# Kernel optimization log

Hardware: AMD Instinct MI355X
Metric: run time of the kernel (lower is better)

## Reference

```python
import jax, jax.numpy as jnp
import numpy as np

TEMPERATURE = 1.0
ITERATIONS = 5


def setup_inputs() -> dict:
    key = jax.random.key(0)
    logits = jax.random.normal(key, (64, 1024, 1024), dtype=jnp.float32)
    return {"logits": logits}


def reference(logits) -> jnp.ndarray:
    # Sinkhorn-Knopp in log space: alternate row and column log-normalization.
    def body(log_alpha, _):
        log_alpha = log_alpha - jax.nn.logsumexp(log_alpha, axis=2, keepdims=True)
        log_alpha = log_alpha - jax.nn.logsumexp(log_alpha, axis=1, keepdims=True)
        return log_alpha, None

    log_alpha, _ = jax.lax.scan(body, logits, None, length=ITERATIONS)
    return jnp.exp(log_alpha / TEMPERATURE)
```

## Files before the change

kernel.cpp:

```cpp
#include <hip/hip_runtime.h>


constexpr int BATCH = 64;
constexpr int N = 1024;
constexpr int ROWS_PER_WAVE = 16;
constexpr int WAVES_PER_WG = 4;
constexpr int PASS_BLOCKS = (BATCH * N) / (ROWS_PER_WAVE * WAVES_PER_WG);
constexpr int FINAL_BLOCKS = 16384;

__global__ __launch_bounds__(256) void init_ws_kernel(float* __restrict__ v,
                                                      float* __restrict__ colsum) {
    int t = blockIdx.x * blockDim.x + threadIdx.x;
    v[t] = 0.0f;
    colsum[t] = 0.0f;
}

__global__ __launch_bounds__(256) void sinkhorn_pass_kernel(
    const float* __restrict__ logits, const float* __restrict__ v,
    float* __restrict__ u, float* __restrict__ colsum) {
    __shared__ float lds[WAVES_PER_WG * N];

    const int tid = threadIdx.x;
    const int lane = tid & 63;
    const int wid = tid >> 6;
    const int wave_g = blockIdx.x * WAVES_PER_WG + wid;
    const int row0 = wave_g * ROWS_PER_WAVE;
    const int b = row0 >> 10;

    const float4* vb = reinterpret_cast<const float4*>(v + (b << 10));
    float4 vr[4];
#pragma unroll
    for (int c = 0; c < 4; ++c) vr[c] = vb[c * 64 + lane];

    float4 acc[4];
#pragma unroll
    for (int c = 0; c < 4; ++c) acc[c] = make_float4(0.f, 0.f, 0.f, 0.f);

    const float4* lb =
        reinterpret_cast<const float4*>(logits) + (size_t)row0 * (N / 4) + lane;

    for (int ii = 0; ii < ROWS_PER_WAVE; ++ii) {
        float4 x[4];
#pragma unroll
        for (int c = 0; c < 4; ++c) x[c] = lb[ii * (N / 4) + c * 64];
#pragma unroll
        for (int c = 0; c < 4; ++c) {
            x[c].x -= vr[c].x;
            x[c].y -= vr[c].y;
            x[c].z -= vr[c].z;
            x[c].w -= vr[c].w;
        }
        float m = x[0].x;
#pragma unroll
        for (int c = 0; c < 4; ++c) {
            m = fmaxf(m, x[c].x);
            m = fmaxf(m, x[c].y);
            m = fmaxf(m, x[c].z);
            m = fmaxf(m, x[c].w);
        }
#pragma unroll
        for (int off = 32; off >= 1; off >>= 1) m = fmaxf(m, __shfl_xor(m, off));
        float s = 0.f;
#pragma unroll
        for (int c = 0; c < 4; ++c) {
            x[c].x = __expf(x[c].x - m); s += x[c].x;
            x[c].y = __expf(x[c].y - m); s += x[c].y;
            x[c].z = __expf(x[c].z - m); s += x[c].z;
            x[c].w = __expf(x[c].w - m); s += x[c].w;
        }
#pragma unroll
        for (int off = 32; off >= 1; off >>= 1) s += __shfl_xor(s, off);
        if (lane == 0) u[row0 + ii] = m + __logf(s);
        const float rinv = __builtin_amdgcn_rcpf(s);
#pragma unroll
        for (int c = 0; c < 4; ++c) {
            acc[c].x = fmaf(x[c].x, rinv, acc[c].x);
            acc[c].y = fmaf(x[c].y, rinv, acc[c].y);
            acc[c].z = fmaf(x[c].z, rinv, acc[c].z);
            acc[c].w = fmaf(x[c].w, rinv, acc[c].w);
        }
    }
#pragma unroll
    for (int c = 0; c < 4; ++c) {
        acc[c].x *= __expf(vr[c].x);
        acc[c].y *= __expf(vr[c].y);
        acc[c].z *= __expf(vr[c].z);
        acc[c].w *= __expf(vr[c].w);
    }
    float4* lw = reinterpret_cast<float4*>(lds + wid * N);
#pragma unroll
    for (int c = 0; c < 4; ++c) lw[c * 64 + lane] = acc[c];
    __syncthreads();

    const int j0 = tid * 4;
    float4 s0 = *reinterpret_cast<const float4*>(lds + 0 * N + j0);
    const float4 s1 = *reinterpret_cast<const float4*>(lds + 1 * N + j0);
    const float4 s2 = *reinterpret_cast<const float4*>(lds + 2 * N + j0);
    const float4 s3 = *reinterpret_cast<const float4*>(lds + 3 * N + j0);
    s0.x += s1.x + s2.x + s3.x;
    s0.y += s1.y + s2.y + s3.y;
    s0.z += s1.z + s2.z + s3.z;
    s0.w += s1.w + s2.w + s3.w;
    float* dst = colsum + (b << 10) + j0;
    atomicAdd(dst + 0, s0.x);
    atomicAdd(dst + 1, s0.y);
    atomicAdd(dst + 2, s0.z);
    atomicAdd(dst + 3, s0.w);
}

__global__ __launch_bounds__(256) void finalize_kernel(float* __restrict__ colsum,
                                                       float* __restrict__ v) {
    int t = blockIdx.x * blockDim.x + threadIdx.x;
    v[t] = __logf(colsum[t]);
    colsum[t] = 0.0f;
}

__global__ __launch_bounds__(256) void final_kernel(const float* __restrict__ logits,
                                                    const float* __restrict__ u,
                                                    const float* __restrict__ v,
                                                    float* __restrict__ out) {
    const int g0 = blockIdx.x * 256 + threadIdx.x;
#pragma unroll
    for (int p = 0; p < 4; ++p) {
        const int g = g0 + p * (FINAL_BLOCKS * 256);
        const int e = g << 2;
        const int r = e >> 10;
        const int jc = e & 1023;
        const int b = r >> 10;
        const float ur = u[r];
        const float4 vv = *reinterpret_cast<const float4*>(v + (b << 10) + jc);
        const float4 x = *reinterpret_cast<const float4*>(logits + (size_t)e);
        float4 o;
        o.x = __expf(x.x - ur - vv.x);
        o.y = __expf(x.y - ur - vv.y);
        o.z = __expf(x.z - ur - vv.z);
        o.w = __expf(x.w - ur - vv.w);
        *reinterpret_cast<float4*>(out + (size_t)e) = o;
    }
}

extern "C" void kernel_launch(void* const* d_in, const int* in_sizes, int n_in,
                              void* d_out, int out_size, void* d_ws, size_t ws_size,
                              hipStream_t stream) {
    const float* logits = (const float*)d_in[0];
    float* out = (float*)d_out;
    float* ws = (float*)d_ws;
    float* u = ws;
    float* v = ws + 65536;
    float* colsum = ws + 131072;

    init_ws_kernel<<<256, 256, 0, stream>>>(v, colsum);
    for (int it = 0; it < 5; ++it) {
        sinkhorn_pass_kernel<<<PASS_BLOCKS, 256, 0, stream>>>(logits, v, u, colsum);
        finalize_kernel<<<256, 256, 0, stream>>>(colsum, v);
    }
    final_kernel<<<FINAL_BLOCKS, 256, 0, stream>>>(logits, u, v, out);
}
```

Measured before the change: 714.8 us.

## Reuse pass-one row max and multiply by reciprocal column sums instead of logs

Measured after the change: 1.135 ms. 1.59x slower.

```diff
diff --git a/kernel.cpp b/kernel.cpp
--- a/kernel.cpp
+++ b/kernel.cpp
@@ -8,16 +8,15 @@
 constexpr int PASS_BLOCKS = (BATCH * N) / (ROWS_PER_WAVE * WAVES_PER_WG);
 constexpr int FINAL_BLOCKS = 16384;
 
-__global__ __launch_bounds__(256) void init_ws_kernel(float* __restrict__ v,
-                                                      float* __restrict__ colsum) {
+__global__ __launch_bounds__(256) void init_ws_kernel(float* __restrict__ cs) {
     int t = blockIdx.x * blockDim.x + threadIdx.x;
-    v[t] = 0.0f;
-    colsum[t] = 0.0f;
+    cs[t] = 0.0f;
 }
 
-__global__ __launch_bounds__(256) void sinkhorn_pass_kernel(
-    const float* __restrict__ logits, const float* __restrict__ v,
-    float* __restrict__ u, float* __restrict__ colsum) {
+template <bool PASS1>
+__global__ __launch_bounds__(256, 4) void sinkhorn_pass_kernel(
+    const float* __restrict__ logits, const float* __restrict__ csprev,
+    float* __restrict__ u, float* __restrict__ rowmax, float* __restrict__ csout) {
     __shared__ float lds[WAVES_PER_WG * N];
 
     const int tid = threadIdx.x;
@@ -27,10 +26,18 @@
     const int row0 = wave_g * ROWS_PER_WAVE;
     const int b = row0 >> 10;
 
-    const float4* vb = reinterpret_cast<const float4*>(v + (b << 10));
-    float4 vr[4];
+    float4 rc[4];
+    if constexpr (!PASS1) {
+        const float4* cb = reinterpret_cast<const float4*>(csprev + (b << 10));
 #pragma unroll
-    for (int c = 0; c < 4; ++c) vr[c] = vb[c * 64 + lane];
+        for (int c = 0; c < 4; ++c) {
+            const float4 cs = cb[c * 64 + lane];
+            rc[c].x = 1.0f / cs.x;
+            rc[c].y = 1.0f / cs.y;
+            rc[c].z = 1.0f / cs.z;
+            rc[c].w = 1.0f / cs.w;
+        }
+    }
 
     float4 acc[4];
 #pragma unroll
@@ -39,54 +46,71 @@
     const float4* lb =
         reinterpret_cast<const float4*>(logits) + (size_t)row0 * (N / 4) + lane;
 
-    for (int ii = 0; ii < ROWS_PER_WAVE; ++ii) {
-        float4 x[4];
+    auto LOADR = [&](float4* X, int r) {
 #pragma unroll
-        for (int c = 0; c < 4; ++c) x[c] = lb[ii * (N / 4) + c * 64];
+        for (int c = 0; c < 4; ++c) X[c] = lb[r * (N / 4) + c * 64];
+    };
+
+    auto PROCESS = [&](float4* X, int r) {
+        float mh;
+        if constexpr (PASS1) {
+            float m = X[0].x;
+#pragma unroll
+            for (int c = 0; c < 4; ++c) {
+                m = fmaxf(m, fmaxf(fmaxf(X[c].x, X[c].y), fmaxf(X[c].z, X[c].w)));
+            }
+#pragma unroll
+            for (int off = 32; off >= 1; off >>= 1) m = fmaxf(m, __shfl_xor(m, off));
+            mh = m;
+        } else {
+            mh = rowmax[row0 + r];
+        }
+        float4 sv = make_float4(0.f, 0.f, 0.f, 0.f);
 #pragma unroll
         for (int c = 0; c < 4; ++c) {
-            x[c].x -= vr[c].x;
-            x[c].y -= vr[c].y;
-            x[c].z -= vr[c].z;
-            x[c].w -= vr[c].w;
+            X[c].x = __expf(X[c].x - mh);
+            X[c].y = __expf(X[c].y - mh);
+            X[c].z = __expf(X[c].z - mh);
+            X[c].w = __expf(X[c].w - mh);
+            if constexpr (PASS1) {
+                sv.x += X[c].x;
+                sv.y += X[c].y;
+                sv.z += X[c].z;
+                sv.w += X[c].w;
+            } else {
+                sv.x = fmaf(X[c].x, rc[c].x, sv.x);
+                sv.y = fmaf(X[c].y, rc[c].y, sv.y);
+                sv.z = fmaf(X[c].z, rc[c].z, sv.z);
+                sv.w = fmaf(X[c].w, rc[c].w, sv.w);
+            }
         }
-        float m = x[0].x;
-#pragma unroll
-        for (int c = 0; c < 4; ++c) {
-            m = fmaxf(m, x[c].x);
-            m = fmaxf(m, x[c].y);
-            m = fmaxf(m, x[c].z);
-            m = fmaxf(m, x[c].w);
-        }
-#pragma unroll
-        for (int off = 32; off >= 1; off >>= 1) m = fmaxf(m, __shfl_xor(m, off));
-        float s = 0.f;
-#pragma unroll
-        for (int c = 0; c < 4; ++c) {
-            x[c].x = __expf(x[c].x - m); s += x[c].x;
-            x[c].y = __expf(x[c].y - m); s += x[c].y;
-            x[c].z = __expf(x[c].z - m); s += x[c].z;
-            x[c].w = __expf(x[c].w - m); s += x[c].w;
-        }
+        float s = (sv.x + sv.y) + (sv.z + sv.w);
 #pragma unroll
         for (int off = 32; off >= 1; off >>= 1) s += __shfl_xor(s, off);
-        if (lane == 0) u[row0 + ii] = m + __logf(s);
+        if (lane == 0) {
+            u[row0 + r] = mh + __logf(s);
+            if constexpr (PASS1) rowmax[row0 + r] = mh;
+        }
         const float rinv = __builtin_amdgcn_rcpf(s);
 #pragma unroll
         for (int c = 0; c < 4; ++c) {
-            acc[c].x = fmaf(x[c].x, rinv, acc[c].x);
-            acc[c].y = fmaf(x[c].y, rinv, acc[c].y);
-            acc[c].z = fmaf(x[c].z, rinv, acc[c].z);
-            acc[c].w = fmaf(x[c].w, rinv, acc[c].w);
+            acc[c].x = fmaf(X[c].x, rinv, acc[c].x);
+            acc[c].y = fmaf(X[c].y, rinv, acc[c].y);
+            acc[c].z = fmaf(X[c].z, rinv, acc[c].z);
+            acc[c].w = fmaf(X[c].w, rinv, acc[c].w);
         }
+    };
+
+    float4 A[4], B[4];
+    LOADR(A, 0);
+#pragma unroll
+    for (int r = 0; r < ROWS_PER_WAVE; r += 2) {
+        LOADR(B, r + 1);
+        PROCESS(A, r);
+        if (r + 2 < ROWS_PER_WAVE) LOADR(A, r + 2);
+        PROCESS(B, r + 1);
     }
-#pragma unroll
-    for (int c = 0; c < 4; ++c) {
-        acc[c].x *= __expf(vr[c].x);
-        acc[c].y *= __expf(vr[c].y);
-        acc[c].z *= __expf(vr[c].z);
-        acc[c].w *= __expf(vr[c].w);
-    }
+
     float4* lw = reinterpret_cast<float4*>(lds + wid * N);
 #pragma unroll
     for (int c = 0; c < 4; ++c) lw[c * 64 + lane] = acc[c];
@@ -101,18 +125,17 @@
     s0.y += s1.y + s2.y + s3.y;
     s0.z += s1.z + s2.z + s3.z;
     s0.w += s1.w + s2.w + s3.w;
-    float* dst = colsum + (b << 10) + j0;
+    float* dst = csout + (b << 10) + j0;
     atomicAdd(dst + 0, s0.x);
     atomicAdd(dst + 1, s0.y);
     atomicAdd(dst + 2, s0.z);
     atomicAdd(dst + 3, s0.w);
 }
 
-__global__ __launch_bounds__(256) void finalize_kernel(float* __restrict__ colsum,
+__global__ __launch_bounds__(256) void finalize_kernel(const float* __restrict__ cs,
                                                        float* __restrict__ v) {
     int t = blockIdx.x * blockDim.x + threadIdx.x;
-    v[t] = __logf(colsum[t]);
-    colsum[t] = 0.0f;
+    v[t] = __logf(cs[t]);
 }
 
 __global__ __launch_bounds__(256) void final_kernel(const float* __restrict__ logits,
@@ -146,13 +169,17 @@
     float* out = (float*)d_out;
     float* ws = (float*)d_ws;
     float* u = ws;
-    float* v = ws + 65536;
-    float* colsum = ws + 131072;
+    float* rowmax = ws + 65536;
+    float* v = ws + 2 * 65536;
+    float* cs = ws + 3 * 65536;
 
-    init_ws_kernel<<<256, 256, 0, stream>>>(v, colsum);
-    for (int it = 0; it < 5; ++it) {
-        sinkhorn_pass_kernel<<<PASS_BLOCKS, 256, 0, stream>>>(logits, v, u, colsum);
-        finalize_kernel<<<256, 256, 0, stream>>>(colsum, v);
+    init_ws_kernel<<<1280, 256, 0, stream>>>(cs);
+    sinkhorn_pass_kernel<true><<<PASS_BLOCKS, 256, 0, stream>>>(logits, cs, u, rowmax,
+                                                                cs);
+    for (int it = 1; it < 5; ++it) {
+        sinkhorn_pass_kernel<false><<<PASS_BLOCKS, 256, 0, stream>>>(
+            logits, cs + (it - 1) * 65536, u, rowmax, cs + it * 65536);
     }
+    finalize_kernel<<<256, 256, 0, stream>>>(cs + 4 * 65536, v);
     final_kernel<<<FINAL_BLOCKS, 256, 0, stream>>>(logits, u, v, out);
 }
```
